# Performance work log

Measured on AMD Instinct MI355X. Metric: run time of the kernel, lower is better.

## Reference

```python
import jax, jax.numpy as jnp
import numpy as np

B, H, T, D = 4, 16, 2048, 64


def setup_inputs() -> dict:
    key = jax.random.key(0)
    kq, kk, kv = jax.random.split(key, 3)
    q = jax.random.normal(kq, (B, H, T, D), dtype=jnp.float32)
    k = jax.random.normal(kk, (B, H, T, D), dtype=jnp.float32)
    v = jax.random.normal(kv, (B, H, T, D), dtype=jnp.float32)
    return {"q": q, "k": k, "v": v}


def reference(q, k, v):
    # scores: [B,H,T,T] = q @ k^T (no softmax, linear attention)
    scores = jnp.einsum("bhtd,bhsd->bhts", q, k)
    # causal multiplicative mask: lower-triangular ones (zero out future keys)
    t = q.shape[-2]
    causal = jnp.tril(jnp.ones((t, t), dtype=scores.dtype))  # [T,T]
    scores = scores * causal  # broadcast over [B,H]
    # output: [B,H,T,D] = masked_scores @ v
    return jnp.einsum("bhts,bhsd->bhtd", scores, v)
```

## Files before the change

kernel.cpp:

```cpp
#include <hip/hip_runtime.h>
#include <hip/hip_bf16.h>


#define B_   4
#define H_   16
#define T_   2048
#define D_   64
#define BH_  64
#define CCH  256
#define NCH  8
#define LPAD 8
#define LW   (D_ + LPAD)

typedef __bf16 bf16x4 __attribute__((ext_vector_type(4)));
typedef __bf16 bf16x8 __attribute__((ext_vector_type(8)));
typedef float  f32x2  __attribute__((ext_vector_type(2)));
typedef float  f32x4  __attribute__((ext_vector_type(4)));


__global__ __launch_bounds__(256, 2) void kv_chunk_kernel(
    const float* __restrict__ k, const float* __restrict__ v,
    float* __restrict__ kvws) {
  __shared__ __align__(16) __bf16 KT[2][D_][LW];
  __shared__ __align__(16) __bf16 VT[2][D_][LW];

  const int tid  = threadIdx.x;
  const int lane = tid & 63;
  const int w    = tid >> 6;
  const int quad = lane >> 4;
  const int l15  = lane & 15;
  const int bh   = blockIdx.x >> 3;
  const int c    = blockIdx.x & (NCH - 1);
  const long base = ((long)bh * T_ + (long)c * CCH) * D_;

  const int s4 = tid >> 4;
  const int d4 = tid & 15;

  f32x4 kreg[4], vreg[4];
  const float* kp0 = k + base + (long)(s4 * 4) * D_ + d4 * 4;
  const float* vp0 = v + base + (long)(s4 * 4) * D_ + d4 * 4;

  auto LOAD = [&](int st) {
#pragma unroll
    for (int r = 0; r < 4; ++r) {
      kreg[r] = *(const f32x4*)(kp0 + (long)(st * 64 + r) * D_);
      vreg[r] = *(const f32x4*)(vp0 + (long)(st * 64 + r) * D_);
    }
  };
  auto WRITE = [&](int p) {
#pragma unroll
    for (int cc2 = 0; cc2 < 4; ++cc2) {
      bf16x4 ka, va;
#pragma unroll
      for (int r = 0; r < 4; ++r) {
        ka[r] = (__bf16)kreg[r][cc2];
        va[r] = (__bf16)vreg[r][cc2];
      }
      *(bf16x4*)&KT[p][d4 * 4 + cc2][s4 * 4] = ka;
      *(bf16x4*)&VT[p][d4 * 4 + cc2][s4 * 4] = va;
    }
  };

  const f32x4 vzero = {0.f, 0.f, 0.f, 0.f};
  f32x4 acc[4];
#pragma unroll
  for (int n = 0; n < 4; ++n) acc[n] = vzero;

  LOAD(0);
  WRITE(0);
  __syncthreads();
  for (int st = 0; st < 4; ++st) {
    const int p = st & 1;
    if (st < 3) LOAD(st + 1);
#pragma unroll
    for (int ks = 0; ks < 2; ++ks) {
      bf16x8 a = *(const bf16x8*)&KT[p][w * 16 + l15][ks * 32 + quad * 8];
#pragma unroll
      for (int n = 0; n < 4; ++n) {
        bf16x8 b = *(const bf16x8*)&VT[p][n * 16 + l15][ks * 32 + quad * 8];
        acc[n] = __builtin_amdgcn_mfma_f32_16x16x32_bf16(a, b, acc[n], 0, 0, 0);
      }
    }
    if (st < 3) {
      WRITE(p ^ 1);
      __syncthreads();
    }
  }
  float* out = kvws + ((long)blockIdx.x << 12);
#pragma unroll
  for (int n = 0; n < 4; ++n)
#pragma unroll
    for (int rr = 0; rr < 4; ++rr)
      out[(w * 16 + quad * 4 + rr) * 64 + n * 16 + l15] = acc[n][rr];
}

__global__ __launch_bounds__(512, 4) void attn_chunk_kernel(
    const float* __restrict__ q, const float* __restrict__ k,
    const float* __restrict__ v, const float* __restrict__ kvws,
    float* __restrict__ out) {
  __shared__ __align__(16) __bf16 KVT[D_][LW];
  __shared__ __align__(16) __bf16 Kj[2][64][LW];
  __shared__ __align__(16) __bf16 VTj[2][D_][LW];
  __shared__ __align__(16) __bf16 Sw[8][16][LW];

  const int tid  = threadIdx.x;
  const int lane = tid & 63;
  const int w    = tid >> 6;
  const int quad = lane >> 4;
  const int l15  = lane & 15;
  const int bh   = blockIdx.x >> 3;
  const int c    = blockIdx.x & (NCH - 1);
  const long base = ((long)bh * T_ + (long)c * CCH) * D_;

  const int slK = tid >> 3;
  const int d0K = (tid & 7) * 8;
  const int sV  = (tid >> 5) * 4;
  const int dV  = (tid & 31) * 2;

  f32x4 kreg0, kreg1;
  f32x2 vreg[4];
  auto LOADJ = [&](int j) {
    const float* kp = k + base + (long)(j * 64 + slK) * D_ + d0K;
    const float* vp = v + base + (long)(j * 64 + sV) * D_ + dV;
    kreg0 = *(const f32x4*)(kp);
    kreg1 = *(const f32x4*)(kp + 4);
#pragma unroll
    for (int r = 0; r < 4; ++r) vreg[r] = *(const f32x2*)(vp + (long)r * D_);
  };
  auto WRITEJ = [&](int p) {
    bf16x8 kb;
#pragma unroll
    for (int e = 0; e < 4; ++e) {
      kb[e]     = (__bf16)kreg0[e];
      kb[4 + e] = (__bf16)kreg1[e];
    }
    *(bf16x8*)&Kj[p][slK][d0K] = kb;
#pragma unroll
    for (int e = 0; e < 2; ++e) {
      bf16x4 va;
#pragma unroll
      for (int r = 0; r < 4; ++r) va[r] = (__bf16)vreg[r][e];
      *(bf16x4*)&VTj[p][dV + e][sV] = va;
    }
  };

  float kvacc[8];
#pragma unroll
  for (int i = 0; i < 8; ++i) kvacc[i] = 0.f;
  const float* wsbh = kvws + ((long)(bh * NCH) << 12);
  for (int cc = 0; cc < c; ++cc) {
    const float* pp = wsbh + ((long)cc << 12) + tid * 8;
#pragma unroll
    for (int x = 0; x < 2; ++x) {
      f32x4 t = *(const f32x4*)(pp + x * 4);
#pragma unroll
      for (int e = 0; e < 4; ++e) kvacc[x * 4 + e] += t[e];
    }
  }
  {
    const int d1  = tid >> 3;
    const int d2b = (tid & 7) * 8;
#pragma unroll
    for (int ii = 0; ii < 8; ++ii) KVT[d2b + ii][d1] = (__bf16)kvacc[ii];
  }

  bf16x8 qf[2][2];
#pragma unroll
  for (int t = 0; t < 2; ++t) {
    const int m = t ? (15 - w) : w;
    const int row = m * 16 + l15;
    const float* qp = q + base + (long)row * D_ + quad * 8;
#pragma unroll
    for (int ks = 0; ks < 2; ++ks) {
      f32x4 lo = *(const f32x4*)(qp + ks * 32);
      f32x4 hi = *(const f32x4*)(qp + ks * 32 + 4);
      bf16x8 f;
#pragma unroll
      for (int e = 0; e < 4; ++e) {
        f[e]     = (__bf16)lo[e];
        f[4 + e] = (__bf16)hi[e];
      }
      qf[t][ks] = f;
    }
  }

  const f32x4 vzero = {0.f, 0.f, 0.f, 0.f};
  f32x4 acc[2][4];
#pragma unroll
  for (int t = 0; t < 2; ++t)
#pragma unroll
    for (int n = 0; n < 4; ++n) acc[t][n] = vzero;

  LOADJ(0);
  WRITEJ(0);
  __syncthreads();
  LOADJ(1);

#pragma unroll
  for (int ks = 0; ks < 2; ++ks)
#pragma unroll
    for (int n = 0; n < 4; ++n) {
      bf16x8 b = *(const bf16x8*)&KVT[n * 16 + l15][ks * 32 + quad * 8];
#pragma unroll
      for (int t = 0; t < 2; ++t)
        acc[t][n] =
            __builtin_amdgcn_mfma_f32_16x16x32_bf16(qf[t][ks], b, acc[t][n], 0, 0, 0);
    }

  for (int j = 0; j < 4; ++j) {
    const int p = j & 1;
#pragma unroll
    for (int t = 0; t < 2; ++t) {
      const int m = t ? (15 - w) : w;
      if (m >= 4 * j) {
        f32x4 s[4];
#pragma unroll
        for (int n = 0; n < 4; ++n) s[n] = vzero;
#pragma unroll
        for (int ks = 0; ks < 2; ++ks)
#pragma unroll
          for (int n = 0; n < 4; ++n) {
            bf16x8 kf = *(const bf16x8*)&Kj[p][n * 16 + l15][ks * 32 + quad * 8];
            s[n] = __builtin_amdgcn_mfma_f32_16x16x32_bf16(kf, qf[t][ks], s[n],
                                                           0, 0, 0);
          }
        const int mloc = (m & 3) * 16;
        const bool diag = ((m >> 2) == j);
#pragma unroll
        for (int n = 0; n < 4; ++n) {
          bf16x4 pk;
#pragma unroll
          for (int rr = 0; rr < 4; ++rr) {
            float val = s[n][rr];
            if (diag && (n * 16 + quad * 4 + rr > mloc + l15)) val = 0.f;
            pk[rr] = (__bf16)val;
          }
          *(bf16x4*)&Sw[w][l15][n * 16 + quad * 4] = pk;
        }
#pragma unroll
        for (int ks = 0; ks < 2; ++ks) {
          bf16x8 a = *(const bf16x8*)&Sw[w][l15][ks * 32 + quad * 8];
#pragma unroll
          for (int n = 0; n < 4; ++n) {
            bf16x8 vf = *(const bf16x8*)&VTj[p][n * 16 + l15][ks * 32 + quad * 8];
            acc[t][n] =
                __builtin_amdgcn_mfma_f32_16x16x32_bf16(a, vf, acc[t][n], 0, 0, 0);
          }
        }
      }
    }
    if (j < 3) {
      WRITEJ(p ^ 1);
      __syncthreads();
      if (j < 2) LOADJ(j + 2);
    }
  }

  float* op = out + base;
#pragma unroll
  for (int t = 0; t < 2; ++t) {
    const int m = t ? (15 - w) : w;
    const int row = m * 16 + quad * 4;
#pragma unroll
    for (int n = 0; n < 4; ++n)
#pragma unroll
      for (int rr = 0; rr < 4; ++rr)
        op[(long)(row + rr) * D_ + n * 16 + l15] = acc[t][n][rr];
  }
}

extern "C" void kernel_launch(void* const* d_in, const int* in_sizes, int n_in,
                              void* d_out, int out_size, void* d_ws, size_t ws_size,
                              hipStream_t stream) {
  const float* q = (const float*)d_in[0];
  const float* k = (const float*)d_in[1];
  const float* v = (const float*)d_in[2];
  float* out = (float*)d_out;
  float* kvws = (float*)d_ws;

  hipLaunchKernelGGL(kv_chunk_kernel, dim3(BH_ * NCH), dim3(256), 0, stream,
                     k, v, kvws);
  hipLaunchKernelGGL(attn_chunk_kernel, dim3(BH_ * NCH), dim3(512), 0, stream,
                     q, k, v, kvws, out);
}
```

Measured before the change: 146.5 us.

## Fuse KV chunk-state and attention kernels with flag-based inter-block sync

```diff
diff --git a/kernel.cpp b/kernel.cpp
--- a/kernel.cpp
+++ b/kernel.cpp
@@ -12,105 +12,59 @@
 #define LPAD 8
 #define LW   (D_ + LPAD)
 
+#define FLAG_OFF_BYTES (8u << 20)
+
 typedef __bf16 bf16x4 __attribute__((ext_vector_type(4)));
 typedef __bf16 bf16x8 __attribute__((ext_vector_type(8)));
 typedef float  f32x2  __attribute__((ext_vector_type(2)));
 typedef float  f32x4  __attribute__((ext_vector_type(4)));
 
 
-__global__ __launch_bounds__(256, 2) void kv_chunk_kernel(
-    const float* __restrict__ k, const float* __restrict__ v,
-    float* __restrict__ kvws) {
-  __shared__ __align__(16) __bf16 KT[2][D_][LW];
-  __shared__ __align__(16) __bf16 VT[2][D_][LW];
+__global__ __launch_bounds__(512, 4) void fused_attn_kernel(
+    const float* __restrict__ q, const float* __restrict__ k,
+    const float* __restrict__ v, float* __restrict__ kvws,
+    int* __restrict__ flags, float* __restrict__ out) {
+  __shared__ __align__(16) __bf16 KVT[D_][LW];
+  __shared__ __align__(16) __bf16 Kj[2][64][LW];
+  __shared__ __align__(16) __bf16 VTj[2][64][LW];
+  __shared__ __align__(16) __bf16 Sw[8][16][LW];
 
   const int tid  = threadIdx.x;
   const int lane = tid & 63;
   const int w    = tid >> 6;
   const int quad = lane >> 4;
   const int l15  = lane & 15;
-  const int bh   = blockIdx.x >> 3;
-  const int c    = blockIdx.x & (NCH - 1);
+  const int bx  = blockIdx.x;
+  const int bh  = (bx & 7) * 8 + ((bx >> 3) & 7);
+  const int c   = bx >> 6;
+  const int lin = bh * NCH + c;
   const long base = ((long)bh * T_ + (long)c * CCH) * D_;
 
-  const int s4 = tid >> 4;
-  const int d4 = tid & 15;
-
-  f32x4 kreg[4], vreg[4];
-  const float* kp0 = k + base + (long)(s4 * 4) * D_ + d4 * 4;
-  const float* vp0 = v + base + (long)(s4 * 4) * D_ + d4 * 4;
-
-  auto LOAD = [&](int st) {
-#pragma unroll
-    for (int r = 0; r < 4; ++r) {
-      kreg[r] = *(const f32x4*)(kp0 + (long)(st * 64 + r) * D_);
-      vreg[r] = *(const f32x4*)(vp0 + (long)(st * 64 + r) * D_);
-    }
-  };
-  auto WRITE = [&](int p) {
+  const f32x4 vzero = {0.f, 0.f, 0.f, 0.f};
+
+  const int tt  = tid & 255;
+  const int s4a = tt >> 4;
+  const int d4a = tt & 15;
+  const int mat = tid >> 8;
+  const float* src1 = mat ? v : k;
+  __bf16* dst1 = mat ? &VTj[0][0][0] : &Kj[0][0][0];
+  const float* sp1 = src1 + base + (long)(s4a * 4) * D_ + d4a * 4;
+
+  f32x4 reg1[4];
+  auto LOAD1 = [&](int st) {
+#pragma unroll
+    for (int r = 0; r < 4; ++r)
+      reg1[r] = *(const f32x4*)(sp1 + (long)(st * 64 + r) * D_);
+  };
+  auto WRITE1 = [&](int p) {
 #pragma unroll
     for (int cc2 = 0; cc2 < 4; ++cc2) {
-      bf16x4 ka, va;
-#pragma unroll
-      for (int r = 0; r < 4; ++r) {
-        ka[r] = (__bf16)kreg[r][cc2];
-        va[r] = (__bf16)vreg[r][cc2];
-      }
-      *(bf16x4*)&KT[p][d4 * 4 + cc2][s4 * 4] = ka;
-      *(bf16x4*)&VT[p][d4 * 4 + cc2][s4 * 4] = va;
-    }
-  };
-
-  const f32x4 vzero = {0.f, 0.f, 0.f, 0.f};
-  f32x4 acc[4];
-#pragma unroll
-  for (int n = 0; n < 4; ++n) acc[n] = vzero;
-
-  LOAD(0);
-  WRITE(0);
-  __syncthreads();
-  for (int st = 0; st < 4; ++st) {
-    const int p = st & 1;
-    if (st < 3) LOAD(st + 1);
-#pragma unroll
-    for (int ks = 0; ks < 2; ++ks) {
-      bf16x8 a = *(const bf16x8*)&KT[p][w * 16 + l15][ks * 32 + quad * 8];
-#pragma unroll
-      for (int n = 0; n < 4; ++n) {
-        bf16x8 b = *(const bf16x8*)&VT[p][n * 16 + l15][ks * 32 + quad * 8];
-        acc[n] = __builtin_amdgcn_mfma_f32_16x16x32_bf16(a, b, acc[n], 0, 0, 0);
-      }
-    }
-    if (st < 3) {
-      WRITE(p ^ 1);
-      __syncthreads();
-    }
-  }
-  float* out = kvws + ((long)blockIdx.x << 12);
-#pragma unroll
-  for (int n = 0; n < 4; ++n)
-#pragma unroll
-    for (int rr = 0; rr < 4; ++rr)
-      out[(w * 16 + quad * 4 + rr) * 64 + n * 16 + l15] = acc[n][rr];
-}
-
-__global__ __launch_bounds__(512, 4) void attn_chunk_kernel(
-    const float* __restrict__ q, const float* __restrict__ k,
-    const float* __restrict__ v, const float* __restrict__ kvws,
-    float* __restrict__ out) {
-  __shared__ __align__(16) __bf16 KVT[D_][LW];
-  __shared__ __align__(16) __bf16 Kj[2][64][LW];
-  __shared__ __align__(16) __bf16 VTj[2][D_][LW];
-  __shared__ __align__(16) __bf16 Sw[8][16][LW];
-
-  const int tid  = threadIdx.x;
-  const int lane = tid & 63;
-  const int w    = tid >> 6;
-  const int quad = lane >> 4;
-  const int l15  = lane & 15;
-  const int bh   = blockIdx.x >> 3;
-  const int c    = blockIdx.x & (NCH - 1);
-  const long base = ((long)bh * T_ + (long)c * CCH) * D_;
+      bf16x4 a;
+#pragma unroll
+      for (int r = 0; r < 4; ++r) a[r] = (__bf16)reg1[r][cc2];
+      *(bf16x4*)(dst1 + ((long)p * 64 + d4a * 4 + cc2) * LW + s4a * 4) = a;
+    }
+  };
 
   const int slK = tid >> 3;
   const int d0K = (tid & 7) * 8;
@@ -144,32 +98,14 @@
     }
   };
 
-  float kvacc[8];
-#pragma unroll
-  for (int i = 0; i < 8; ++i) kvacc[i] = 0.f;
-  const float* wsbh = kvws + ((long)(bh * NCH) << 12);
-  for (int cc = 0; cc < c; ++cc) {
-    const float* pp = wsbh + ((long)cc << 12) + tid * 8;
-#pragma unroll
-    for (int x = 0; x < 2; ++x) {
-      f32x4 t = *(const f32x4*)(pp + x * 4);
-#pragma unroll
-      for (int e = 0; e < 4; ++e) kvacc[x * 4 + e] += t[e];
-    }
-  }
-  {
-    const int d1  = tid >> 3;
-    const int d2b = (tid & 7) * 8;
-#pragma unroll
-    for (int ii = 0; ii < 8; ++ii) KVT[d2b + ii][d1] = (__bf16)kvacc[ii];
-  }
+  LOAD1(0);
+  WRITE1(0);
 
   bf16x8 qf[2][2];
 #pragma unroll
   for (int t = 0; t < 2; ++t) {
     const int m = t ? (15 - w) : w;
-    const int row = m * 16 + l15;
-    const float* qp = q + base + (long)row * D_ + quad * 8;
+    const float* qp = q + base + (long)(m * 16 + l15) * D_ + quad * 8;
 #pragma unroll
     for (int ks = 0; ks < 2; ++ks) {
       f32x4 lo = *(const f32x4*)(qp + ks * 32);
@@ -184,17 +120,74 @@
     }
   }
 
-  const f32x4 vzero = {0.f, 0.f, 0.f, 0.f};
-  f32x4 acc[2][4];
-#pragma unroll
-  for (int t = 0; t < 2; ++t)
-#pragma unroll
-    for (int n = 0; n < 4; ++n) acc[t][n] = vzero;
+  __syncthreads();
+
+  const int r1 = (w & 3) * 16;
+  const int nb = (w >> 2) * 2;
+  f32x4 acc1[2] = {vzero, vzero};
+  for (int st = 0; st < 4; ++st) {
+    const int p = st & 1;
+    if (st < 3) LOAD1(st + 1);
+#pragma unroll
+    for (int ks = 0; ks < 2; ++ks) {
+      bf16x8 a = *(const bf16x8*)&Kj[p][r1 + l15][ks * 32 + quad * 8];
+#pragma unroll
+      for (int nn = 0; nn < 2; ++nn) {
+        bf16x8 b = *(const bf16x8*)&VTj[p][(nb + nn) * 16 + l15][ks * 32 + quad * 8];
+        acc1[nn] = __builtin_amdgcn_mfma_f32_16x16x32_bf16(a, b, acc1[nn], 0, 0, 0);
+      }
+    }
+    if (st < 3) {
+      WRITE1(p ^ 1);
+      __syncthreads();
+    }
+  }
+  {
+    float* wsp = kvws + ((long)lin << 12);
+#pragma unroll
+    for (int nn = 0; nn < 2; ++nn)
+#pragma unroll
+      for (int rr = 0; rr < 4; ++rr)
+        wsp[(r1 + quad * 4 + rr) * 64 + (nb + nn) * 16 + l15] = acc1[nn][rr];
+  }
+  __syncthreads();
+  if (tid == 0)
+    __hip_atomic_store(&flags[lin], 1, __ATOMIC_RELEASE, __HIP_MEMORY_SCOPE_AGENT);
 
   LOADJ(0);
   WRITEJ(0);
+
+  float kvacc[8];
+#pragma unroll
+  for (int i = 0; i < 8; ++i) kvacc[i] = 0.f;
+  const float* wsbh = kvws + ((long)(bh * NCH) << 12);
+  for (int cc = 0; cc < c; ++cc) {
+    while (__hip_atomic_load(&flags[bh * NCH + cc], __ATOMIC_ACQUIRE,
+                             __HIP_MEMORY_SCOPE_AGENT) == 0)
+      __builtin_amdgcn_s_sleep(2);
+    const float* pp = wsbh + ((long)cc << 12) + tid * 8;
+#pragma unroll
+    for (int x = 0; x < 2; ++x) {
+      f32x4 t2 = *(const f32x4*)(pp + x * 4);
+#pragma unroll
+      for (int e = 0; e < 4; ++e) kvacc[x * 4 + e] += t2[e];
+    }
+  }
+  {
+    const int d1  = tid >> 3;
+    const int d2b = (tid & 7) * 8;
+#pragma unroll
+    for (int ii = 0; ii < 8; ++ii) KVT[d2b + ii][d1] = (__bf16)kvacc[ii];
+  }
+
+  f32x4 acc[2][4];
+#pragma unroll
+  for (int t = 0; t < 2; ++t)
+#pragma unroll
+    for (int n = 0; n < 4; ++n) acc[t][n] = vzero;
+
+  LOADJ(1);
   __syncthreads();
-  LOADJ(1);
 
 #pragma unroll
   for (int ks = 0; ks < 2; ++ks)
@@ -209,6 +202,7 @@
 
   for (int j = 0; j < 4; ++j) {
     const int p = j & 1;
+    __builtin_amdgcn_s_setprio(1);
 #pragma unroll
     for (int t = 0; t < 2; ++t) {
       const int m = t ? (15 - w) : w;
@@ -249,6 +243,7 @@
         }
       }
     }
+    __builtin_amdgcn_s_setprio(0);
     if (j < 3) {
       WRITEJ(p ^ 1);
       __syncthreads();
@@ -277,9 +272,9 @@
   const float* v = (const float*)d_in[2];
   float* out = (float*)d_out;
   float* kvws = (float*)d_ws;
-
-  hipLaunchKernelGGL(kv_chunk_kernel, dim3(BH_ * NCH), dim3(256), 0, stream,
-                     k, v, kvws);
-  hipLaunchKernelGGL(attn_chunk_kernel, dim3(BH_ * NCH), dim3(512), 0, stream,
-                     q, k, v, kvws, out);
+  int* flags = (int*)((char*)d_ws + FLAG_OFF_BYTES);
+
+  hipMemsetAsync(flags, 0, BH_ * NCH * sizeof(int), stream);
+  hipLaunchKernelGGL(fused_attn_kernel, dim3(BH_ * NCH), dim3(512), 0, stream,
+                     q, k, v, kvws, flags, out);
 }
```

After: 270.6 us. 1.85x slower.
